# Kernel optimization log

Hardware: AMD Instinct MI355X
Metric: run time of the kernel (lower is better)

## Reference

```python
import jax, jax.numpy as jnp
import numpy as np

V = 50257   # input_size (vocab)
H = 1024    # hidden_size
LZ = 128    # latent_size
CD = 32     # conditional_size
L = 256     # sequence length
SOS = 0


def _lstm_cell(x, h, c, W_ih, W_hh, b_ih, b_hh):
    # PyTorch LSTM gate order: i, f, g, o
    g = x @ W_ih.T + h @ W_hh.T + b_ih + b_hh  # [4H]
    i, f, gg, o = jnp.split(g, 4, axis=-1)
    c = jax.nn.sigmoid(f) * c + jax.nn.sigmoid(i) * jnp.tanh(gg)
    h = jax.nn.sigmoid(o) * jnp.tanh(c)
    return h, c


def setup_inputs() -> dict:
    key = jax.random.key(0)
    ks = jax.random.split(key, 24)
    s = 0.02
    n = lambda k, shp: (s * jax.random.normal(k, shp)).astype(jnp.float32)
    return {
        "input_tensor": jax.random.randint(ks[0], (L, 1), 0, V, dtype=jnp.int32),
        "encoder_hidden_state": jnp.zeros((1, 1, H), jnp.float32),
        "encoder_cell_state": jnp.zeros((1, 1, H), jnp.float32),
        "c": jax.random.normal(ks[1], (1, 1, CD), dtype=jnp.float32),
        "use_teacher_forcing": 1,
        "enc_emb": n(ks[2], (V, H)),
        "enc_W_ih": n(ks[3], (4 * H, H)),
        "enc_W_hh": n(ks[4], (4 * H, H)),
        "enc_b_ih": jnp.zeros((4 * H,), jnp.float32),
        "enc_b_hh": jnp.zeros((4 * H,), jnp.float32),
        "dec_emb": n(ks[5], (V, H)),
        "dec_W_ih": n(ks[6], (4 * H, H)),
        "dec_W_hh": n(ks[7], (4 * H, H)),
        "dec_b_ih": jnp.zeros((4 * H,), jnp.float32),
        "dec_b_hh": jnp.zeros((4 * H,), jnp.float32),
        "out_W": n(ks[8], (V, H)),
        "out_b": jnp.zeros((V,), jnp.float32),
        "mean_W": n(ks[9], (LZ, H)),
        "mean_b": jnp.zeros((LZ,), jnp.float32),
        "logvar_W": n(ks[10], (LZ, H)),
        "logvar_b": jnp.zeros((LZ,), jnp.float32),
        "lc_W": n(ks[11], (H, LZ + CD)),
        "lc_b": jnp.zeros((H,), jnp.float32),
    }


def reference(input_tensor, encoder_hidden_state, encoder_cell_state, c,
              use_teacher_forcing,
              enc_emb, enc_W_ih, enc_W_hh, enc_b_ih, enc_b_hh,
              dec_emb, dec_W_ih, dec_W_hh, dec_b_ih, dec_b_hh,
              out_W, out_b, mean_W, mean_b, logvar_W, logvar_b, lc_W, lc_b):
    tokens = input_tensor[:, 0]  # [L] int

    # ---- encoder: sequential LSTM over embedded tokens ----
    x_seq = enc_emb[tokens]  # [L, H]
    h0 = encoder_hidden_state.reshape(H)
    c0 = encoder_cell_state.reshape(H)

    def enc_step(carry, x):
        h, cc = _lstm_cell(x, carry[0], carry[1], enc_W_ih, enc_W_hh, enc_b_ih, enc_b_hh)
        return (h, cc), None
    (h_enc, _), _ = jax.lax.scan(enc_step, (h0, c0), x_seq)

    # ---- middle: reparameterization + latent+condition -> decoder hidden ----
    h_enc3 = h_enc.reshape(1, 1, H)
    mean = h_enc3 @ mean_W.T + mean_b        # [1,1,LZ]
    logvar = h_enc3 @ logvar_W.T + logvar_b  # [1,1,LZ]
    eps = jax.random.normal(jax.random.key(1), mean.shape, dtype=mean.dtype)
    latent = mean + eps * jnp.exp(0.5 * logvar)
    dec_h = (jnp.concatenate([latent, c], axis=-1) @ lc_W.T + lc_b).reshape(H)
    dec_c = jnp.zeros((H,), dec_h.dtype)

    # ---- decoder with teacher forcing: inputs = [SOS, tok_0, ..., tok_{L-2}] ----
    dec_tokens = jnp.concatenate([jnp.array([SOS], dtype=tokens.dtype), tokens[:-1]])
    dec_x = jax.nn.relu(dec_emb[dec_tokens])  # [L, H]

    def dec_step(carry, x):
        h, cc = _lstm_cell(x, carry[0], carry[1], dec_W_ih, dec_W_hh, dec_b_ih, dec_b_hh)
        logits = h @ out_W.T + out_b           # [V]
        return (h, cc), jax.nn.log_softmax(logits)
    _, predict_distribution = jax.lax.scan(dec_step, (dec_h, dec_c), dec_x)  # [L, V]

    predict_output = jnp.argmax(predict_distribution, axis=1).astype(jnp.int32)[:, None]  # [L,1]
    return predict_output, predict_distribution, mean, logvar


if __name__ == "__main__":
    out = reference(**setup_inputs())
    print([o.shape for o in out])
```

## Files before the change

kernel.cpp:

```cpp
#include <hip/hip_runtime.h>
#include <math.h>

#define VOCAB 50257
#define HID   1024
#define G4    4096
#define LZD   128
#define CDD   32
#define SEQ   256
#define NWG   256
#define DECTAG 300u

typedef unsigned long long ull;

__device__ __forceinline__ float sigm(float x){ return 1.0f/(1.0f+expf(-x)); }

__device__ __forceinline__ void pub_val(ull* p, float x, unsigned tag){
  ull v = ((ull)tag<<32) | (ull)__float_as_uint(x);
  __hip_atomic_store(p, v, __ATOMIC_RELAXED, __HIP_MEMORY_SCOPE_AGENT);
}
__device__ __forceinline__ ull ald(ull* p){
  return __hip_atomic_load(p, __ATOMIC_RELAXED, __HIP_MEMORY_SCOPE_AGENT);
}
__device__ __forceinline__ float poll_val(ull* p, unsigned tag){
  ull v = ald(p);
  while((unsigned)(v>>32) != tag){ __builtin_amdgcn_s_sleep(1); v = ald(p); }
  return __uint_as_float((unsigned)v);
}
__device__ __forceinline__ void poll4(ull* slot, float* hb, int tid, unsigned tag){
  ull *p0=&slot[tid], *p1=&slot[tid+256], *p2=&slot[tid+512], *p3=&slot[tid+768];
  ull v0=ald(p0), v1=ald(p1), v2=ald(p2), v3=ald(p3);
  for(;;){
    const bool o0=((unsigned)(v0>>32)==tag), o1=((unsigned)(v1>>32)==tag);
    const bool o2=((unsigned)(v2>>32)==tag), o3=((unsigned)(v3>>32)==tag);
    if(o0 & o1 & o2 & o3) break;
    __builtin_amdgcn_s_sleep(1);
    if(!o0) v0=ald(p0);
    if(!o1) v1=ald(p1);
    if(!o2) v2=ald(p2);
    if(!o3) v3=ald(p3);
  }
  hb[tid]     = __uint_as_float((unsigned)v0);
  hb[tid+256] = __uint_as_float((unsigned)v1);
  hb[tid+512] = __uint_as_float((unsigned)v2);
  hb[tid+768] = __uint_as_float((unsigned)v3);
}

__device__ __forceinline__ float eps_from_bits(unsigned bits){
  float f = __uint_as_float((bits>>9) | 0x3F800000u) - 1.0f;
  const float MINV = -0.99999994f;
  float u = fmaxf(MINV, f*2.0f + MINV);
  float w = -log1pf(-u*u);
  float p;
  if(w < 5.0f){
    w -= 2.5f;
    p =  2.81022636e-08f;
    p = fmaf(p,w, 3.43273939e-07f);
    p = fmaf(p,w,-3.5233877e-06f);
    p = fmaf(p,w,-4.39150654e-06f);
    p = fmaf(p,w, 0.00021858087f);
    p = fmaf(p,w,-0.00125372503f);
    p = fmaf(p,w,-0.00417768164f);
    p = fmaf(p,w, 0.246640727f);
    p = fmaf(p,w, 1.50140941f);
  }else{
    w = sqrtf(w) - 3.0f;
    p = -0.000200214257f;
    p = fmaf(p,w, 0.000100950558f);
    p = fmaf(p,w, 0.00134934322f);
    p = fmaf(p,w,-0.00367342844f);
    p = fmaf(p,w, 0.00573950773f);
    p = fmaf(p,w,-0.0076224613f);
    p = fmaf(p,w, 0.00943887047f);
    p = fmaf(p,w, 1.00167406f);
    p = fmaf(p,w, 2.83297682f);
  }
  return 1.4142135623730951f * (p*u);
}

__global__ __launch_bounds__(256) void vae_embed(
    const int* __restrict__ tok, const float* __restrict__ enc_emb,
    const float* __restrict__ dec_emb,
    float* __restrict__ xenc, float* __restrict__ xdec, ull* __restrict__ tags)
{
  const int b = blockIdx.x, tid = threadIdx.x;
  if(b == SEQ){
    for(int i=tid; i<2*HID+2*LZD+LZD+CDD; i+=256)
      __hip_atomic_store(&tags[i], 0ULL, __ATOMIC_RELAXED, __HIP_MEMORY_SCOPE_AGENT);
    return;
  }
  const int te = tok[b];
  const int td = (b==0) ? 0 : tok[b-1];
  float4 v = *(const float4*)(enc_emb + (size_t)te*HID + tid*4);
  *(float4*)(xenc + (size_t)b*HID + tid*4) = v;
  float4 u = *(const float4*)(dec_emb + (size_t)td*HID + tid*4);
  u.x=fmaxf(u.x,0.f); u.y=fmaxf(u.y,0.f); u.z=fmaxf(u.z,0.f); u.w=fmaxf(u.w,0.f);
  *(float4*)(xdec + (size_t)b*HID + tid*4) = u;
}

__global__ __launch_bounds__(256) void gemm_pre(
    const float* __restrict__ xe, const float* __restrict__ Wihe,
    const float* __restrict__ be1, const float* __restrict__ be2,
    const float* __restrict__ xd, const float* __restrict__ Wihd,
    const float* __restrict__ bd1, const float* __restrict__ bd2,
    float* __restrict__ preE, float* __restrict__ preD)
{
  const int z = blockIdx.z;
  const float* A  = z ? xd   : xe;
  const float* B  = z ? Wihd : Wihe;
  const float* b1 = z ? bd1  : be1;
  const float* b2 = z ? bd2  : be2;
  float* C        = z ? preD : preE;
  const int K = HID, N = G4;

  __shared__ float As[16*68];
  __shared__ float Bs[16*68];
  const int tid = threadIdx.x;
  const int bn = blockIdx.x<<6, bm = blockIdx.y<<6;
  const int lr = tid>>2, lc4 = (tid&3)<<2;
  const int tx = tid&15, ty = tid>>4;
  const float* Arow = A + (size_t)(bm+lr)*K + lc4;
  const float* Brow = B + (size_t)(bn+lr)*K + lc4;
  float acc[4][4] = {};
  for(int kt=0; kt<K; kt+=16){
    float4 av = *(const float4*)(Arow + kt);
    float4 bv = *(const float4*)(Brow + kt);
    __syncthreads();
    As[(lc4+0)*68+lr]=av.x; As[(lc4+1)*68+lr]=av.y; As[(lc4+2)*68+lr]=av.z; As[(lc4+3)*68+lr]=av.w;
    Bs[(lc4+0)*68+lr]=bv.x; Bs[(lc4+1)*68+lr]=bv.y; Bs[(lc4+2)*68+lr]=bv.z; Bs[(lc4+3)*68+lr]=bv.w;
    __syncthreads();
#pragma unroll
    for(int k=0;k<16;++k){
      float4 a = *(const float4*)(As + k*68 + (ty<<2));
      float4 b = *(const float4*)(Bs + k*68 + (tx<<2));
      float a4[4] = {a.x,a.y,a.z,a.w};
      float b4[4] = {b.x,b.y,b.z,b.w};
#pragma unroll
      for(int i=0;i<4;++i)
#pragma unroll
        for(int j=0;j<4;++j)
          acc[i][j] = fmaf(a4[i], b4[j], acc[i][j]);
    }
  }
  const int n0 = bn + (tx<<2);
#pragma unroll
  for(int i=0;i<4;++i){
    const int m = bm + (ty<<2) + i;
#pragma unroll
    for(int j=0;j<4;++j){
      const int n = n0+j;
      C[(size_t)m*N + n] = acc[i][j] + b1[n] + b2[n];
    }
  }
}

__global__ __launch_bounds__(256) void gemm_nt_128(
    const float* __restrict__ A, const float* __restrict__ B,
    const float* __restrict__ bias, float* __restrict__ C, int K, int N)
{
  __shared__ float As[8][132];
  __shared__ float Bs[8][132];
  const int tid = threadIdx.x;
  const int bn = blockIdx.x<<7, bm = blockIdx.y<<7;
  const int tx = tid&15, ty = tid>>4;
  const int lr = tid>>1, lc = (tid&1)<<2;
  const float* Arow = A + (size_t)(bm+lr)*K + lc;
  const float* Brow = B + (size_t)(bn+lr)*K + lc;
  const bool bval = (bn+lr) < N;
  float4 av = *(const float4*)(Arow);
  float4 bv = bval ? *(const float4*)(Brow) : make_float4(0.f,0.f,0.f,0.f);
  float acc[8][8] = {};
  for(int kt=0; kt<K; kt+=8){
    __syncthreads();
    As[lc+0][lr]=av.x; As[lc+1][lr]=av.y; As[lc+2][lr]=av.z; As[lc+3][lr]=av.w;
    Bs[lc+0][lr]=bv.x; Bs[lc+1][lr]=bv.y; Bs[lc+2][lr]=bv.z; Bs[lc+3][lr]=bv.w;
    __syncthreads();
    if(kt+8 < K){
      av = *(const float4*)(Arow + kt + 8);
      bv = bval ? *(const float4*)(Brow + kt + 8) : make_float4(0.f,0.f,0.f,0.f);
    }
#pragma unroll
    for(int k=0;k<8;++k){
      float a8[8], b8[8];
      *(float4*)(a8)   = *(const float4*)(&As[k][ty*8]);
      *(float4*)(a8+4) = *(const float4*)(&As[k][ty*8+4]);
      *(float4*)(b8)   = *(const float4*)(&Bs[k][tx*8]);
      *(float4*)(b8+4) = *(const float4*)(&Bs[k][tx*8+4]);
#pragma unroll
      for(int i=0;i<8;++i)
#pragma unroll
        for(int j=0;j<8;++j)
          acc[i][j] = fmaf(a8[i], b8[j], acc[i][j]);
    }
  }
  const int m0 = bm + ty*8, n0 = bn + tx*8;
#pragma unroll
  for(int i=0;i<8;++i){
#pragma unroll
    for(int j=0;j<8;++j){
      const int n = n0+j;
      if(n < N) C[(size_t)(m0+i)*N + n] = acc[i][j] + bias[n];
    }
  }
}

__global__ __launch_bounds__(256,1) void vae_scan(
    const float* __restrict__ enc_Whh, const float* __restrict__ dec_Whh,
    const float* __restrict__ pre_enc, const float* __restrict__ pre_dec,
    const float* __restrict__ h0in, const float* __restrict__ c0in,
    const float* __restrict__ ccond,
    const float* __restrict__ mean_W, const float* __restrict__ mean_b,
    const float* __restrict__ logvar_W, const float* __restrict__ logvar_b,
    const float* __restrict__ lc_W, const float* __restrict__ lc_b,
    ull* __restrict__ h_tag, ull* __restrict__ mlv_tag, ull* __restrict__ lat_tag,
    float* __restrict__ Hdec, float* __restrict__ out_mean, float* __restrict__ out_logvar)
{
  __shared__ float W_lds[16*1024];
  __shared__ float h_lds[HID];
  __shared__ float lat_lds[LZD+CDD];
  __shared__ float sh_mlv[2*LZD];
  __shared__ float gbuf[16];
  __shared__ float redb[4];

  const int q = blockIdx.x, tid = threadIdx.x;
  const int g = tid>>4, l = tid&15;
  const int gate = g&3, ul = g>>2;
  const int u4 = 4*q;

  for(int r=0;r<16;++r){
    const float* src = enc_Whh + ((size_t)((r&3)*HID + u4 + (r>>2)))*HID;
    *(float4*)(&W_lds[r*1024 + tid*4]) = *(const float4*)(src + tid*4);
  }
  float creg = (tid<4) ? c0in[u4+tid] : 0.0f;

  for(int t=0; t<SEQ; ++t){
    float pv = 0.f;
    if(l==0) pv = pre_enc[(size_t)t*G4 + gate*HID + u4 + ul];
    if(t==0){
#pragma unroll
      for(int j=0;j<4;++j) h_lds[tid+j*256] = h0in[tid+j*256];
    }else{
      poll4(h_tag + (t&1)*HID, h_lds, tid, (unsigned)t);
    }
    __syncthreads();
    float a0=0,a1=0,a2=0,a3=0;
    {
      const float* wr = &W_lds[g*1024 + l*4];
      const float* hr = &h_lds[l*4];
#pragma unroll
      for(int kk=0; kk<16; ++kk){
        float4 wv = *(const float4*)(wr + kk*64);
        float4 hv = *(const float4*)(hr + kk*64);
        a0 = fmaf(wv.x, hv.x, a0);
        a1 = fmaf(wv.y, hv.y, a1);
        a2 = fmaf(wv.z, hv.z, a2);
        a3 = fmaf(wv.w, hv.w, a3);
      }
    }
    float s = (a0+a1)+(a2+a3);
    s += __shfl_xor(s,1); s += __shfl_xor(s,2); s += __shfl_xor(s,4); s += __shfl_xor(s,8);
    if(l==0) gbuf[g] = s + pv;
    __syncthreads();
    if(tid<4){
      float gi=gbuf[tid*4+0], gf=gbuf[tid*4+1], gg=gbuf[tid*4+2], go=gbuf[tid*4+3];
      float cn = sigm(gf)*creg + sigm(gi)*tanhf(gg);
      float hn = sigm(go)*tanhf(cn);
      creg = cn;
      pub_val(&h_tag[((t+1)&1)*HID + u4+tid], hn, (unsigned)(t+1));
    }
  }

  {
    poll4(h_tag, h_lds, tid, (unsigned)SEQ);
    __syncthreads();
    const float* Wrow = (q < LZD) ? (mean_W + (size_t)q*HID)
                                  : (logvar_W + (size_t)(q-LZD)*HID);
    const float bias = (q < LZD) ? mean_b[q] : logvar_b[q-LZD];
    float4 hv = *(const float4*)(h_lds + tid*4);
    float4 wv = *(const float4*)(Wrow + tid*4);
    float p = hv.x*wv.x + hv.y*wv.y + hv.z*wv.z + hv.w*wv.w;
    p += __shfl_xor(p,1); p += __shfl_xor(p,2); p += __shfl_xor(p,4);
    p += __shfl_xor(p,8); p += __shfl_xor(p,16); p += __shfl_xor(p,32);
    if((tid&63)==0) redb[tid>>6] = p;
    __syncthreads();
    if(tid==0){
      float s = redb[0]+redb[1]+redb[2]+redb[3] + bias;
      pub_val(&mlv_tag[q], s, 1u);
      if(q < LZD) out_mean[q] = s; else out_logvar[q-LZD] = s;
    }
  }

  if(q==0){
    sh_mlv[tid] = poll_val(&mlv_tag[tid], 1u);
    __syncthreads();
    if(tid < LZD){
      unsigned x0 = 0u, x1 = (unsigned)tid;
      const unsigned ks[3] = {0u, 1u, 0x1BD11BDAu ^ 0u ^ 1u};
      x0 += ks[0]; x1 += ks[1];
      const int RA[4] = {13,15,26,6}, RB[4] = {17,29,16,24};
#pragma unroll
      for(int gg2=0; gg2<5; ++gg2){
        const int* R = (gg2&1) ? RB : RA;
#pragma unroll
        for(int qq=0;qq<4;++qq){
          x0 += x1;
          x1 = (x1 << R[qq]) | (x1 >> (32-R[qq]));
          x1 ^= x0;
        }
        x0 += ks[(gg2+1)%3];
        x1 += ks[(gg2+2)%3] + (unsigned)(gg2+1);
      }
      float e = eps_from_bits(x0 ^ x1);
      pub_val(&lat_tag[tid], fmaf(e, expf(0.5f*sh_mlv[LZD+tid]), sh_mlv[tid]), 1u);
    } else if(tid < LZD+CDD){
      pub_val(&lat_tag[tid], ccond[tid-LZD], 1u);
    }
  }

  for(int r=0;r<16;++r){
    const float* src = dec_Whh + ((size_t)((r&3)*HID + u4 + (r>>2)))*HID;
    *(float4*)(&W_lds[r*1024 + tid*4]) = *(const float4*)(src + tid*4);
  }
  if(tid < LZD+CDD) lat_lds[tid] = poll_val(&lat_tag[tid], 1u);
  __syncthreads();
  if(tid<4){
    const int j = u4 + tid;
    float s = lc_b[j];
    const float* wr = lc_W + (size_t)j*(LZD+CDD);
#pragma unroll 8
    for(int k=0;k<LZD+CDD;++k) s = fmaf(lat_lds[k], wr[k], s);
    creg = 0.0f;
    pub_val(&h_tag[j], s, DECTAG);
  }

  for(int t=0; t<SEQ; ++t){
    float pv = 0.f;
    if(l==0) pv = pre_dec[(size_t)t*G4 + gate*HID + u4 + ul];
    poll4(h_tag + (t&1)*HID, h_lds, tid, DECTAG + (unsigned)t);
    __syncthreads();
    float a0=0,a1=0,a2=0,a3=0;
    {
      const float* wr = &W_lds[g*1024 + l*4];
      const float* hr = &h_lds[l*4];
#pragma unroll
      for(int kk=0; kk<16; ++kk){
        float4 wv = *(const float4*)(wr + kk*64);
        float4 hv = *(const float4*)(hr + kk*64);
        a0 = fmaf(wv.x, hv.x, a0);
        a1 = fmaf(wv.y, hv.y, a1);
        a2 = fmaf(wv.z, hv.z, a2);
        a3 = fmaf(wv.w, hv.w, a3);
      }
    }
    float s = (a0+a1)+(a2+a3);
    s += __shfl_xor(s,1); s += __shfl_xor(s,2); s += __shfl_xor(s,4); s += __shfl_xor(s,8);
    if(l==0) gbuf[g] = s + pv;
    __syncthreads();
    if(tid<4){
      float gi=gbuf[tid*4+0], gf=gbuf[tid*4+1], gg=gbuf[tid*4+2], go=gbuf[tid*4+3];
      float cn = sigm(gf)*creg + sigm(gi)*tanhf(gg);
      float hn = sigm(go)*tanhf(cn);
      creg = cn;
      Hdec[(size_t)t*HID + u4 + tid] = hn;
      pub_val(&h_tag[((t+1)&1)*HID + u4+tid], hn, DECTAG + (unsigned)(t+1));
    }
  }
}

__global__ __launch_bounds__(256) void softmax_argmax(float* __restrict__ dist,
                                                      float* __restrict__ outTok)
{
  __shared__ float wm[4]; __shared__ int wi[4];
  __shared__ float s_max; __shared__ int s_idx; __shared__ float s_lz;
  const int t = blockIdx.x, tid = threadIdx.x;
  float* row = dist + (size_t)t*VOCAB;
  float m = -INFINITY; int idx = VOCAB;
  for(int i=tid; i<VOCAB; i+=256){
    float v = row[i];
    if(v > m){ m = v; idx = i; }
  }
  for(int d=1; d<64; d<<=1){
    float m2 = __shfl_xor(m, d); int i2 = __shfl_xor(idx, d);
    if(m2 > m || (m2 == m && i2 < idx)){ m = m2; idx = i2; }
  }
  if((tid&63)==0){ wm[tid>>6]=m; wi[tid>>6]=idx; }
  __syncthreads();
  if(tid==0){
    float mm = wm[0]; int ii = wi[0];
    for(int q=1;q<4;++q) if(wm[q]>mm || (wm[q]==mm && wi[q]<ii)){ mm=wm[q]; ii=wi[q]; }
    s_max = mm; s_idx = ii;
  }
  __syncthreads();
  const float M = s_max;
  float s = 0.f;
  for(int i=tid; i<VOCAB; i+=256) s += expf(row[i] - M);
  for(int d=1; d<64; d<<=1) s += __shfl_xor(s, d);
  if((tid&63)==0) wm[tid>>6] = s;
  __syncthreads();
  if(tid==0) s_lz = M + logf(wm[0]+wm[1]+wm[2]+wm[3]);
  __syncthreads();
  const float lz = s_lz;
  for(int i=tid; i<VOCAB; i+=256) row[i] -= lz;
  if(tid==0) outTok[t] = (float)s_idx;
}

extern "C" void kernel_launch(void* const* d_in, const int* in_sizes, int n_in,
                              void* d_out, int out_size, void* d_ws, size_t ws_size,
                              hipStream_t stream)
{
  (void)in_sizes; (void)n_in; (void)out_size; (void)ws_size;
  const int*   tok      = (const int*)  d_in[0];
  const float* h0       = (const float*)d_in[1];
  const float* c0       = (const float*)d_in[2];
  const float* ccond    = (const float*)d_in[3];
  const float* enc_emb  = (const float*)d_in[5];
  const float* enc_Wih  = (const float*)d_in[6];
  const float* enc_Whh  = (const float*)d_in[7];
  const float* enc_bih  = (const float*)d_in[8];
  const float* enc_bhh  = (const float*)d_in[9];
  const float* dec_emb  = (const float*)d_in[10];
  const float* dec_Wih  = (const float*)d_in[11];
  const float* dec_Whh  = (const float*)d_in[12];
  const float* dec_bih  = (const float*)d_in[13];
  const float* dec_bhh  = (const float*)d_in[14];
  const float* out_W    = (const float*)d_in[15];
  const float* out_b    = (const float*)d_in[16];
  const float* mean_W   = (const float*)d_in[17];
  const float* mean_b   = (const float*)d_in[18];
  const float* logvar_W = (const float*)d_in[19];
  const float* logvar_b = (const float*)d_in[20];
  const float* lc_W     = (const float*)d_in[21];
  const float* lc_b     = (const float*)d_in[22];

  float* ws      = (float*)d_ws;
  float* xenc    = ws;
  float* xdec    = xenc + SEQ*HID;
  float* pre_enc = xdec + SEQ*HID;
  float* pre_dec = pre_enc + (size_t)SEQ*G4;
  float* Hdec    = pre_dec + (size_t)SEQ*G4;
  ull*   tags    = (ull*)(Hdec + (size_t)SEQ*HID);
  ull*   h_tag   = tags;
  ull*   mlv_tag = h_tag + 2*HID;
  ull*   lat_tag = mlv_tag + 2*LZD;

  float* out      = (float*)d_out;
  float* outTok   = out;
  float* dist     = out + SEQ;
  float* out_mean = dist + (size_t)SEQ*VOCAB;
  float* out_lv   = out_mean + LZD;

  hipLaunchKernelGGL(vae_embed, dim3(SEQ+1), dim3(256), 0, stream,
                     tok, enc_emb, dec_emb, xenc, xdec, tags);
  hipLaunchKernelGGL(gemm_pre, dim3(G4/64, SEQ/64, 2), dim3(256), 0, stream,
                     xenc, enc_Wih, enc_bih, enc_bhh,
                     xdec, dec_Wih, dec_bih, dec_bhh, pre_enc, pre_dec);
  hipLaunchKernelGGL(vae_scan, dim3(NWG), dim3(256), 0, stream,
                     enc_Whh, dec_Whh, pre_enc, pre_dec, h0, c0, ccond,
                     mean_W, mean_b, logvar_W, logvar_b, lc_W, lc_b,
                     h_tag, mlv_tag, lat_tag, Hdec, out_mean, out_lv);
  hipLaunchKernelGGL(gemm_nt_128, dim3((VOCAB+127)/128, SEQ/128), dim3(256), 0, stream,
                     Hdec, out_W, out_b, dist, HID, VOCAB);
  hipLaunchKernelGGL(softmax_argmax, dim3(SEQ), dim3(256), 0, stream, dist, outTok);
}
```

Measured before the change: 1.866 ms.

## Use split-bf16 MFMA for the output logits GEMM

Replaces the FP32 SIMT output-projection GEMM (256x50257x1024) with a matrix-core version. Each FP32 operand is split into high and low bf16 parts, and the product is accumulated with three bf16 MFMAs (hi*hi, hi*lo, lo*hi) to keep near-FP32 accuracy. The aim is to move the large logits GEMM off the vector ALUs and onto the MFMA units. In exchange it adds per-tile conversion work and unpipelined global loads, and accuracy is slightly below full FP32.

Result: faster. 1.747 ms (-6.4%).

```diff
diff --git a/kernel.cpp b/kernel.cpp
--- a/kernel.cpp
+++ b/kernel.cpp
@@ -11,8 +11,19 @@
 #define DECTAG 300u
 
 typedef unsigned long long ull;
+typedef __attribute__((ext_vector_type(8))) short bf16x8;
+typedef __attribute__((ext_vector_type(4))) float f32x4;
 
 __device__ __forceinline__ float sigm(float x){ return 1.0f/(1.0f+expf(-x)); }
+
+__device__ __forceinline__ unsigned short f2bf(float x){
+  unsigned u = __float_as_uint(x);
+  unsigned r = u + 0x7FFFu + ((u>>16)&1u);
+  return (unsigned short)(r>>16);
+}
+__device__ __forceinline__ float bf2f(unsigned short h){
+  return __uint_as_float(((unsigned)h)<<16);
+}
 
 __device__ __forceinline__ void pub_val(ull* p, float x, unsigned tag){
   ull v = ((ull)tag<<32) | (ull)__float_as_uint(x);
@@ -153,52 +164,75 @@
   }
 }
 
-__global__ __launch_bounds__(256) void gemm_nt_128(
+__global__ __launch_bounds__(256) void gemm_logits_mfma(
     const float* __restrict__ A, const float* __restrict__ B,
     const float* __restrict__ bias, float* __restrict__ C, int K, int N)
 {
-  __shared__ float As[8][132];
-  __shared__ float Bs[8][132];
+  __shared__ unsigned short Ah[128][40], Al[128][40];
+  __shared__ unsigned short Bh[128][40], Bl[128][40];
   const int tid = threadIdx.x;
   const int bn = blockIdx.x<<7, bm = blockIdx.y<<7;
-  const int tx = tid&15, ty = tid>>4;
-  const int lr = tid>>1, lc = (tid&1)<<2;
-  const float* Arow = A + (size_t)(bm+lr)*K + lc;
-  const float* Brow = B + (size_t)(bn+lr)*K + lc;
-  const bool bval = (bn+lr) < N;
-  float4 av = *(const float4*)(Arow);
-  float4 bv = bval ? *(const float4*)(Brow) : make_float4(0.f,0.f,0.f,0.f);
-  float acc[8][8] = {};
-  for(int kt=0; kt<K; kt+=8){
-    __syncthreads();
-    As[lc+0][lr]=av.x; As[lc+1][lr]=av.y; As[lc+2][lr]=av.z; As[lc+3][lr]=av.w;
-    Bs[lc+0][lr]=bv.x; Bs[lc+1][lr]=bv.y; Bs[lc+2][lr]=bv.z; Bs[lc+3][lr]=bv.w;
-    __syncthreads();
-    if(kt+8 < K){
-      av = *(const float4*)(Arow + kt + 8);
-      bv = bval ? *(const float4*)(Brow + kt + 8) : make_float4(0.f,0.f,0.f,0.f);
-    }
-#pragma unroll
-    for(int k=0;k<8;++k){
-      float a8[8], b8[8];
-      *(float4*)(a8)   = *(const float4*)(&As[k][ty*8]);
-      *(float4*)(a8+4) = *(const float4*)(&As[k][ty*8+4]);
-      *(float4*)(b8)   = *(const float4*)(&Bs[k][tx*8]);
-      *(float4*)(b8+4) = *(const float4*)(&Bs[k][tx*8+4]);
-#pragma unroll
-      for(int i=0;i<8;++i)
-#pragma unroll
-        for(int j=0;j<8;++j)
-          acc[i][j] = fmaf(a8[i], b8[j], acc[i][j]);
-    }
-  }
-  const int m0 = bm + ty*8, n0 = bn + tx*8;
-#pragma unroll
-  for(int i=0;i<8;++i){
-#pragma unroll
-    for(int j=0;j<8;++j){
-      const int n = n0+j;
-      if(n < N) C[(size_t)(m0+i)*N + n] = acc[i][j] + bias[n];
+  const int wid = tid>>6, lane = tid&63;
+  const int wr = wid>>1, wc = wid&1;
+  const int l15 = lane&15, l4 = lane>>4;
+  const int sr = tid>>1, sc0 = (tid&1)<<4;
+  const bool bok = (bn+sr) < N;
+  const float* Asrc = A + (size_t)(bm+sr)*K + sc0;
+  const float* Bsrc = B + (size_t)(bn+sr)*K + sc0;
+
+  f32x4 acc[4][4] = {};
+
+  for(int kt=0; kt<K; kt+=32){
+    __syncthreads();
+#pragma unroll
+    for(int j=0;j<16;j+=2){
+      float2 v = *(const float2*)(Asrc + kt + j);
+      unsigned short hx=f2bf(v.x), hy=f2bf(v.y);
+      unsigned short lx=f2bf(v.x - bf2f(hx)), ly=f2bf(v.y - bf2f(hy));
+      *(unsigned*)&Ah[sr][sc0+j] = ((unsigned)hy<<16)|hx;
+      *(unsigned*)&Al[sr][sc0+j] = ((unsigned)ly<<16)|lx;
+    }
+#pragma unroll
+    for(int j=0;j<16;j+=2){
+      float2 v = bok ? *(const float2*)(Bsrc + kt + j) : make_float2(0.f,0.f);
+      unsigned short hx=f2bf(v.x), hy=f2bf(v.y);
+      unsigned short lx=f2bf(v.x - bf2f(hx)), ly=f2bf(v.y - bf2f(hy));
+      *(unsigned*)&Bh[sr][sc0+j] = ((unsigned)hy<<16)|hx;
+      *(unsigned*)&Bl[sr][sc0+j] = ((unsigned)ly<<16)|lx;
+    }
+    __syncthreads();
+    bf16x8 aH[4],aL[4],bH[4],bL[4];
+#pragma unroll
+    for(int f=0; f<4; ++f){
+      const int ar = wr*64 + f*16 + l15;
+      aH[f] = *(const bf16x8*)&Ah[ar][l4*8];
+      aL[f] = *(const bf16x8*)&Al[ar][l4*8];
+      const int br = wc*64 + f*16 + l15;
+      bH[f] = *(const bf16x8*)&Bh[br][l4*8];
+      bL[f] = *(const bf16x8*)&Bl[br][l4*8];
+    }
+#pragma unroll
+    for(int i=0;i<4;++i)
+#pragma unroll
+      for(int j=0;j<4;++j){
+        acc[i][j] = __builtin_amdgcn_mfma_f32_16x16x32_bf16(aH[i], bH[j], acc[i][j], 0,0,0);
+        acc[i][j] = __builtin_amdgcn_mfma_f32_16x16x32_bf16(aH[i], bL[j], acc[i][j], 0,0,0);
+        acc[i][j] = __builtin_amdgcn_mfma_f32_16x16x32_bf16(aL[i], bH[j], acc[i][j], 0,0,0);
+      }
+  }
+
+#pragma unroll
+  for(int i=0;i<4;++i){
+#pragma unroll
+    for(int j=0;j<4;++j){
+      const int col = bn + wc*64 + j*16 + l15;
+      if(col < N){
+        const float bb = bias[col];
+        const int row0 = bm + wr*64 + i*16 + l4*4;
+#pragma unroll
+        for(int r=0;r<4;++r)
+          C[(size_t)(row0+r)*N + col] = acc[i][j][r] + bb;
+      }
     }
   }
 }
@@ -457,7 +491,7 @@
                      enc_Whh, dec_Whh, pre_enc, pre_dec, h0, c0, ccond,
                      mean_W, mean_b, logvar_W, logvar_b, lc_W, lc_b,
                      h_tag, mlv_tag, lat_tag, Hdec, out_mean, out_lv);
-  hipLaunchKernelGGL(gemm_nt_128, dim3((VOCAB+127)/128, SEQ/128), dim3(256), 0, stream,
+  hipLaunchKernelGGL(gemm_logits_mfma, dim3((VOCAB+127)/128, SEQ/128), dim3(256), 0, stream,
                      Hdec, out_W, out_b, dist, HID, VOCAB);
   hipLaunchKernelGGL(softmax_argmax, dim3(SEQ), dim3(256), 0, stream, dist, outTok);
 }
```
